# Optimization experiments

Measured on AMD Instinct MI355X. Metric: run time of the kernel, lower is better.

The kernel has to match this reference:

```python
import jax, jax.numpy as jnp
import numpy as np

IN_DIM = 256
LATENT = 1024
OUT_DIM = 256
B = 128
T = 1024


def setup_inputs() -> dict:
    key = jax.random.key(0)
    k1, k2, k3, k4 = jax.random.split(key, 4)
    # torch Linear weight layout: [out_features, in_features]
    bound_lin = 1.0 / np.sqrt(IN_DIM + LATENT)
    bound_dec = 1.0 / np.sqrt(LATENT)
    return {
        "x": jax.random.normal(k1, (B, T, IN_DIM), dtype=jnp.float32),
        "W_lin": jax.random.uniform(k2, (LATENT, IN_DIM + LATENT), minval=-bound_lin, maxval=bound_lin, dtype=jnp.float32),
        "W_dec": jax.random.uniform(k3, (OUT_DIM, LATENT), minval=-bound_dec, maxval=bound_dec, dtype=jnp.float32),
        "b_dec": jax.random.uniform(k4, (OUT_DIM,), minval=-bound_dec, maxval=bound_dec, dtype=jnp.float32),
    }


def reference(x, W_lin, W_dec, b_dec):
    # cat((x_t, h), dim=1) @ W_lin.T == x_t @ Wx.T + h @ Wh.T
    Wx = W_lin[:, :IN_DIM]      # [latent, in_dim]
    Wh = W_lin[:, IN_DIM:]      # [latent, latent]
    h0 = jnp.zeros((x.shape[0], LATENT), dtype=x.dtype)

    def step(h, x_t):
        h_new = jnp.tanh(x_t @ Wx.T + h @ Wh.T)
        return h_new, None

    # scan over time: x -> [T, B, in_dim]
    h_final, _ = jax.lax.scan(step, h0, jnp.swapaxes(x, 0, 1))
    return jnp.tanh(h_final @ W_dec.T + b_dec)
```

## Files before the change

### kernel.cpp

```cpp
#include <hip/hip_runtime.h>
#include <hip/hip_bf16.h>
#include <stdint.h>

#define B_    128
#define T_    1024
#define IN_   256
#define L_    1024
#define OUT_  256
#define KTOT  1280

#define GROUPS 8
#define WPG    32
#define NB     16
#define NC     32
#define PAD_K  1288
#define LDS_W_BYTES (NC * PAD_K * 2)
#define RED_BYTES   (8 * 4 * 64 * 4)
#define STILE_BYTES (16 * 32 * 2)
#define LDS_TOTAL   (LDS_W_BYTES + RED_BYTES + STILE_BYTES)

#define SENT      0x7F807F80u
#define SLOT      (B_ * L_)
#define RETRY_CAP 200000
#define GAP_MIN   4u
#define GAP_MAX   800u
#define GAP_INIT  16u

using short8 = __attribute__((ext_vector_type(8))) short;
using bf16x8 = __attribute__((ext_vector_type(8))) __bf16;
using f32x4  = __attribute__((ext_vector_type(4))) float;
using u32x4  = __attribute__((ext_vector_type(4))) unsigned;

__device__ __forceinline__ unsigned short f2b(float f) {
  unsigned u = __builtin_bit_cast(unsigned, f);
  u += 0x7FFFu + ((u >> 16) & 1u);
  return (unsigned short)(u >> 16);
}
__device__ __forceinline__ float b2f(unsigned short h) {
  unsigned u = ((unsigned)h) << 16;
  return __builtin_bit_cast(float, u);
}
__device__ __forceinline__ float fast_tanh(float z) {
  z = fminf(fmaxf(z, -30.f), 30.f);
  float e2 = __expf(2.f * z);
  return __fdividef(e2 - 1.f, e2 + 1.f);
}
__device__ __forceinline__ int chunk_ok(short8 c) {
  u32x4 u = __builtin_bit_cast(u32x4, c);
  return (u[0] != SENT) & (u[1] != SENT) & (u[2] != SENT) & (u[3] != SENT);
}
__device__ __forceinline__ void st_dw(unsigned int* p, unsigned int v) {
  asm volatile("global_store_dword %0, %1, off sc1" :: "v"(p), "v"(v) : "memory");
}
__device__ __forceinline__ void ld_x4(short8& d, const unsigned short* p) {
  asm volatile("global_load_dwordx4 %0, %1, off sc1 nt" : "=v"(d) : "v"(p) : "memory");
}

__global__ void init_ws(unsigned int* ring_dw) {
  size_t i = (size_t)blockIdx.x * 256 + threadIdx.x;
  const size_t total = (size_t)4 * SLOT / 2;
  for (size_t k = i; k < total; k += (size_t)256 * 256) ring_dw[k] = SENT;
}

__global__ __launch_bounds__(256, 1)
void rnn_persistent(const float* __restrict__ x, const float* __restrict__ Wlin,
                    unsigned short* __restrict__ ring)
{
  extern __shared__ char smem[];
  short* Wlds = (short*)smem;
  float* red  = (float*)(smem + LDS_W_BYTES);
  unsigned short* stile = (unsigned short*)(smem + LDS_W_BYTES + RED_BYTES);

  const int tid = threadIdx.x;
  const int g   = blockIdx.x & 7;
  const int w   = blockIdx.x >> 3;
  const int bb  = g * NB;
  const int cc  = w * NC;

  for (int r = 0; r < NC; ++r) {
    const float* wrow = Wlin + (size_t)(cc + r) * KTOT;
    for (int k = tid; k < KTOT; k += 256)
      Wlds[r * PAD_K + k] = (short)f2b(wrow[k]);
  }
  __syncthreads();

  const int wv   = tid >> 6;
  const int l    = tid & 63;
  const int lrow = l & 15;
  const int lk   = (l >> 4) * 8;
  const int prow = tid >> 4;
  const int pcol = tid & 15;

  uint64_t pub_ts = 0;
  unsigned gap    = GAP_INIT;

  for (int t = 0; t < T_; ++t) {
    const unsigned short* hcur = ring + (size_t)(t & 3) * SLOT;
    unsigned short*       hnxt = ring + (size_t)((t + 1) & 3) * SLOT;

    if (t >= 2) {
      unsigned int* rp = (unsigned int*)(ring + (size_t)((t + 2) & 3) * SLOT
                                         + (size_t)(bb + prow) * L_ + cc) + pcol;
      st_dw(rp, SENT);
    }

    f32x4 acc0 = {0.f, 0.f, 0.f, 0.f};
    f32x4 acc1 = {0.f, 0.f, 0.f, 0.f};

    #pragma unroll
    for (int j = 0; j < 2; ++j) {
      const int kk    = wv + 4 * j;
      const int kbase = kk * 32 + lk;
      const float* xp = x + ((size_t)(bb + lrow) * T_ + t) * IN_ + kbase;
      f32x4 x0 = *(const f32x4*)xp;
      f32x4 x1 = *(const f32x4*)(xp + 4);
      short8 a;
      a[0] = (short)f2b(x0[0]); a[1] = (short)f2b(x0[1]);
      a[2] = (short)f2b(x0[2]); a[3] = (short)f2b(x0[3]);
      a[4] = (short)f2b(x1[0]); a[5] = (short)f2b(x1[1]);
      a[6] = (short)f2b(x1[2]); a[7] = (short)f2b(x1[3]);
      short8 b0 = *(const short8*)&Wlds[lrow        * PAD_K + kbase];
      short8 b1 = *(const short8*)&Wlds[(lrow + 16) * PAD_K + kbase];
      acc0 = __builtin_amdgcn_mfma_f32_16x16x32_bf16(
               __builtin_bit_cast(bf16x8, a), __builtin_bit_cast(bf16x8, b0), acc0, 0, 0, 0);
      acc1 = __builtin_amdgcn_mfma_f32_16x16x32_bf16(
               __builtin_bit_cast(bf16x8, a), __builtin_bit_cast(bf16x8, b1), acc1, 0, 0, 0);
    }

    if (t > 0) {
      const uint64_t dl = pub_ts + gap;
      while (__builtin_amdgcn_s_memrealtime() < dl)
        __builtin_amdgcn_s_sleep(1);

      const unsigned short* hbase = hcur + (size_t)(bb + lrow) * L_ + wv * 32 + lk;
      short8 hf[8];
      #pragma unroll
      for (int j = 0; j < 8; ++j)
        ld_x4(hf[j], hbase + j * 128);
      asm volatile("s_waitcnt vmcnt(0)" ::: "memory");
      __builtin_amdgcn_sched_barrier(0);

      bool okj[8] = {false, false, false, false, false, false, false, false};
      int remaining = 8, tries = 0;
      while (true) {
        #pragma unroll
        for (int j = 0; j < 8; ++j)
          if (!okj[j] && __all(chunk_ok(hf[j]))) { okj[j] = true; --remaining; }
        if (remaining == 0) break;
        if (++tries > RETRY_CAP) break;
        __builtin_amdgcn_s_sleep(1);
        #pragma unroll
        for (int j = 0; j < 8; ++j)
          if (!okj[j]) ld_x4(hf[j], hbase + j * 128);
        asm volatile("s_waitcnt vmcnt(0)" ::: "memory");
        __builtin_amdgcn_sched_barrier(0);
      }
      if (tries == 0)      gap = (gap > GAP_MIN) ? gap - 1 : gap;
      else { unsigned inc = (unsigned)tries << 3;
             gap = (gap + inc > GAP_MAX) ? GAP_MAX : gap + inc; }

      #pragma unroll
      for (int j = 0; j < 8; ++j) {
        const int kbase = IN_ + wv * 32 + j * 128 + lk;
        short8 b0 = *(const short8*)&Wlds[lrow        * PAD_K + kbase];
        short8 b1 = *(const short8*)&Wlds[(lrow + 16) * PAD_K + kbase];
        acc0 = __builtin_amdgcn_mfma_f32_16x16x32_bf16(
                 __builtin_bit_cast(bf16x8, hf[j]), __builtin_bit_cast(bf16x8, b0), acc0, 0, 0, 0);
        acc1 = __builtin_amdgcn_mfma_f32_16x16x32_bf16(
                 __builtin_bit_cast(bf16x8, hf[j]), __builtin_bit_cast(bf16x8, b1), acc1, 0, 0, 0);
      }
    }

    #pragma unroll
    for (int j = 0; j < 4; ++j) {
      red[((wv * 2 + 0) * 4 + j) * 64 + l] = acc0[j];
      red[((wv * 2 + 1) * 4 + j) * 64 + l] = acc1[j];
    }
    __syncthreads();
    if (wv < 2) {
      const int tile = wv;
      #pragma unroll
      for (int j = 0; j < 4; ++j) {
        float s = red[((0 * 2 + tile) * 4 + j) * 64 + l]
                + red[((1 * 2 + tile) * 4 + j) * 64 + l]
                + red[((2 * 2 + tile) * 4 + j) * 64 + l]
                + red[((3 * 2 + tile) * 4 + j) * 64 + l];
        float hv = fast_tanh(s);
        stile[((l >> 4) * 4 + j) * 32 + tile * 16 + (l & 15)] = f2b(hv);
      }
    }
    __syncthreads();

    {
      unsigned int v = ((const unsigned int*)stile)[tid];
      unsigned int* dp = (unsigned int*)(hnxt + (size_t)(bb + prow) * L_ + cc) + pcol;
      st_dw(dp, v);
    }
    pub_ts = __builtin_amdgcn_s_memrealtime();
  }
}

__global__ __launch_bounds__(256)
void decode_kernel(const unsigned short* __restrict__ hfin,
                   const float* __restrict__ Wdec, const float* __restrict__ bdec,
                   float* __restrict__ out)
{
  __shared__ float hrow[L_];
  const int b = blockIdx.x, tid = threadIdx.x;
  for (int k = tid; k < L_; k += 256)
    hrow[k] = b2f(hfin[b * L_ + k]);
  __syncthreads();
  float s = bdec[tid];
  const float* wr = Wdec + (size_t)tid * L_;
  #pragma unroll 4
  for (int k = 0; k < L_; k += 4) {
    f32x4 wq = *(const f32x4*)(wr + k);
    s += hrow[k] * wq[0] + hrow[k+1] * wq[1] + hrow[k+2] * wq[2] + hrow[k+3] * wq[3];
  }
  out[b * OUT_ + tid] = fast_tanh(s);
}

extern "C" void kernel_launch(void* const* d_in, const int* in_sizes, int n_in,
                              void* d_out, int out_size, void* d_ws, size_t ws_size,
                              hipStream_t stream)
{
  const float* x    = (const float*)d_in[0];
  const float* Wlin = (const float*)d_in[1];
  const float* Wdec = (const float*)d_in[2];
  const float* bdec = (const float*)d_in[3];
  float* out = (float*)d_out;

  unsigned short* ring = (unsigned short*)d_ws;

  hipFuncSetAttribute((const void*)rnn_persistent,
                      hipFuncAttributeMaxDynamicSharedMemorySize, LDS_TOTAL);

  hipLaunchKernelGGL(init_ws, dim3(256), dim3(256), 0, stream,
                     (unsigned int*)ring);
  hipLaunchKernelGGL(rnn_persistent, dim3(GROUPS * WPG), dim3(256), LDS_TOTAL, stream,
                     x, Wlin, ring);
  hipLaunchKernelGGL(decode_kernel, dim3(B_), dim3(256), 0, stream,
                     ring, Wdec, bdec, out);
}
```

Measured before the change: 3.236 ms.

## Overlap h loads with x MFMAs and consume ready chunks while retrying stale ones

Issues the x loads up front, then waits out a fixed short publish gap and issues the h ring loads before doing the x-part MFMAs, so h load latency overlaps the input projection. The polling loop now accumulates MFMAs for each h chunk as soon as it passes the sentinel check and re-fetches only the stale chunks. The adaptive per-block gap is replaced by a constant. Risks: a fixed gap may poll too eagerly and add memory traffic, and the partial vmcnt wait relies on load ordering assumptions.

```diff
diff --git a/kernel.cpp b/kernel.cpp
--- a/kernel.cpp
+++ b/kernel.cpp
@@ -22,9 +22,7 @@
 #define SENT      0x7F807F80u
 #define SLOT      (B_ * L_)
 #define RETRY_CAP 200000
-#define GAP_MIN   4u
-#define GAP_MAX   800u
-#define GAP_INIT  16u
+#define GAP_TICKS 12ull
 
 using short8 = __attribute__((ext_vector_type(8))) short;
 using bf16x8 = __attribute__((ext_vector_type(8))) __bf16;
@@ -54,6 +52,17 @@
 }
 __device__ __forceinline__ void ld_x4(short8& d, const unsigned short* p) {
   asm volatile("global_load_dwordx4 %0, %1, off sc1 nt" : "=v"(d) : "v"(p) : "memory");
+}
+__device__ __forceinline__ void ld_f4(f32x4& d, const float* p) {
+  asm volatile("global_load_dwordx4 %0, %1, off" : "=v"(d) : "v"(p));
+}
+__device__ __forceinline__ short8 cvt8(f32x4 a, f32x4 b) {
+  short8 v;
+  v[0] = (short)f2b(a[0]); v[1] = (short)f2b(a[1]);
+  v[2] = (short)f2b(a[2]); v[3] = (short)f2b(a[3]);
+  v[4] = (short)f2b(b[0]); v[5] = (short)f2b(b[1]);
+  v[6] = (short)f2b(b[2]); v[7] = (short)f2b(b[3]);
+  return v;
 }
 
 __global__ void init_ws(unsigned int* ring_dw) {
@@ -92,7 +101,6 @@
   const int pcol = tid & 15;
 
   uint64_t pub_ts = 0;
-  unsigned gap    = GAP_INIT;
 
   for (int t = 0; t < T_; ++t) {
     const unsigned short* hcur = ring + (size_t)(t & 3) * SLOT;
@@ -104,21 +112,37 @@
       st_dw(rp, SENT);
     }
 
+    f32x4 xr[4];
+    {
+      const float* xp0 = x + ((size_t)(bb + lrow) * T_ + t) * IN_ + (wv * 32 + lk);
+      const float* xp1 = x + ((size_t)(bb + lrow) * T_ + t) * IN_ + ((wv + 4) * 32 + lk);
+      ld_f4(xr[0], xp0); ld_f4(xr[1], xp0 + 4);
+      ld_f4(xr[2], xp1); ld_f4(xr[3], xp1 + 4);
+    }
+
     f32x4 acc0 = {0.f, 0.f, 0.f, 0.f};
     f32x4 acc1 = {0.f, 0.f, 0.f, 0.f};
+    short8 hf[8];
+    const unsigned short* hbase = hcur + (size_t)(bb + lrow) * L_ + wv * 32 + lk;
+
+    if (t > 0) {
+      const uint64_t dl = pub_ts + GAP_TICKS;
+      while (__builtin_amdgcn_s_memrealtime() < dl)
+        __builtin_amdgcn_s_sleep(1);
+      #pragma unroll
+      for (int j = 0; j < 8; ++j)
+        ld_x4(hf[j], hbase + j * 128);
+      asm volatile("s_waitcnt vmcnt(8)" ::: "memory");
+      __builtin_amdgcn_sched_barrier(0);
+    } else {
+      asm volatile("s_waitcnt vmcnt(0)" ::: "memory");
+      __builtin_amdgcn_sched_barrier(0);
+    }
 
     #pragma unroll
     for (int j = 0; j < 2; ++j) {
-      const int kk    = wv + 4 * j;
-      const int kbase = kk * 32 + lk;
-      const float* xp = x + ((size_t)(bb + lrow) * T_ + t) * IN_ + kbase;
-      f32x4 x0 = *(const f32x4*)xp;
-      f32x4 x1 = *(const f32x4*)(xp + 4);
-      short8 a;
-      a[0] = (short)f2b(x0[0]); a[1] = (short)f2b(x0[1]);
-      a[2] = (short)f2b(x0[2]); a[3] = (short)f2b(x0[3]);
-      a[4] = (short)f2b(x1[0]); a[5] = (short)f2b(x1[1]);
-      a[6] = (short)f2b(x1[2]); a[7] = (short)f2b(x1[3]);
+      const int kbase = (wv + 4 * j) * 32 + lk;
+      short8 a = cvt8(xr[2 * j], xr[2 * j + 1]);
       short8 b0 = *(const short8*)&Wlds[lrow        * PAD_K + kbase];
       short8 b1 = *(const short8*)&Wlds[(lrow + 16) * PAD_K + kbase];
       acc0 = __builtin_amdgcn_mfma_f32_16x16x32_bf16(
@@ -128,46 +152,41 @@
     }
 
     if (t > 0) {
-      const uint64_t dl = pub_ts + gap;
-      while (__builtin_amdgcn_s_memrealtime() < dl)
-        __builtin_amdgcn_s_sleep(1);
-
-      const unsigned short* hbase = hcur + (size_t)(bb + lrow) * L_ + wv * 32 + lk;
-      short8 hf[8];
-      #pragma unroll
-      for (int j = 0; j < 8; ++j)
-        ld_x4(hf[j], hbase + j * 128);
       asm volatile("s_waitcnt vmcnt(0)" ::: "memory");
       __builtin_amdgcn_sched_barrier(0);
 
-      bool okj[8] = {false, false, false, false, false, false, false, false};
-      int remaining = 8, tries = 0;
-      while (true) {
+      unsigned pend = 0xFFu;
+      int tries = 0;
+      while (pend) {
+        unsigned newly = 0;
         #pragma unroll
         for (int j = 0; j < 8; ++j)
-          if (!okj[j] && __all(chunk_ok(hf[j]))) { okj[j] = true; --remaining; }
-        if (remaining == 0) break;
-        if (++tries > RETRY_CAP) break;
-        __builtin_amdgcn_s_sleep(1);
+          if ((pend >> j) & 1u)
+            if (__all(chunk_ok(hf[j]))) newly |= 1u << j;
+        const unsigned still = pend & ~newly;
+        if (still) {
+          #pragma unroll
+          for (int j = 0; j < 8; ++j)
+            if ((still >> j) & 1u) ld_x4(hf[j], hbase + j * 128);
+        }
         #pragma unroll
         for (int j = 0; j < 8; ++j)
-          if (!okj[j]) ld_x4(hf[j], hbase + j * 128);
-        asm volatile("s_waitcnt vmcnt(0)" ::: "memory");
-        __builtin_amdgcn_sched_barrier(0);
-      }
-      if (tries == 0)      gap = (gap > GAP_MIN) ? gap - 1 : gap;
-      else { unsigned inc = (unsigned)tries << 3;
-             gap = (gap + inc > GAP_MAX) ? GAP_MAX : gap + inc; }
-
-      #pragma unroll
-      for (int j = 0; j < 8; ++j) {
-        const int kbase = IN_ + wv * 32 + j * 128 + lk;
-        short8 b0 = *(const short8*)&Wlds[lrow        * PAD_K + kbase];
-        short8 b1 = *(const short8*)&Wlds[(lrow + 16) * PAD_K + kbase];
-        acc0 = __builtin_amdgcn_mfma_f32_16x16x32_bf16(
-                 __builtin_bit_cast(bf16x8, hf[j]), __builtin_bit_cast(bf16x8, b0), acc0, 0, 0, 0);
-        acc1 = __builtin_amdgcn_mfma_f32_16x16x32_bf16(
-                 __builtin_bit_cast(bf16x8, hf[j]), __builtin_bit_cast(bf16x8, b1), acc1, 0, 0, 0);
+          if ((newly >> j) & 1u) {
+            const int kbase = IN_ + wv * 32 + j * 128 + lk;
+            short8 b0 = *(const short8*)&Wlds[lrow        * PAD_K + kbase];
+            short8 b1 = *(const short8*)&Wlds[(lrow + 16) * PAD_K + kbase];
+            acc0 = __builtin_amdgcn_mfma_f32_16x16x32_bf16(
+                     __builtin_bit_cast(bf16x8, hf[j]), __builtin_bit_cast(bf16x8, b0), acc0, 0, 0, 0);
+            acc1 = __builtin_amdgcn_mfma_f32_16x16x32_bf16(
+                     __builtin_bit_cast(bf16x8, hf[j]), __builtin_bit_cast(bf16x8, b1), acc1, 0, 0, 0);
+          }
+        pend = still;
+        if (pend) {
+          if (++tries > RETRY_CAP) break;
+          __builtin_amdgcn_s_sleep(1);
+          asm volatile("s_waitcnt vmcnt(0)" ::: "memory");
+          __builtin_amdgcn_sched_barrier(0);
+        }
       }
     }
 
```

New measurement: 3.971 ms. 1.23x slower.
